# Performance work log

Hardware: AMD Instinct MI355X
Metric: run time of the kernel (lower is better)

## Reference

```python
import jax, jax.numpy as jnp
import numpy as np

B, N, H, E = 16, 10000, 128, 320000


def setup_inputs() -> dict:
    key = jax.random.key(0)
    k1, k2, k3, k4, k5 = jax.random.split(key, 5)
    node_embeddings = jax.random.normal(k1, (B, N, H), dtype=jnp.float32)
    missing_mask = jax.random.randint(k2, (B, N), 0, 2, dtype=jnp.int32)
    edge_index = jax.random.randint(k3, (2, E), 0, N, dtype=jnp.int32)
    W1 = jax.random.normal(k4, (2 * H, H), dtype=jnp.float32) * 0.02
    b1 = jnp.zeros((H,), dtype=jnp.float32)
    W2 = jax.random.normal(k5, (H, H), dtype=jnp.float32) * 0.02
    b2 = jnp.zeros((H,), dtype=jnp.float32)
    return {"node_embeddings": node_embeddings, "missing_mask": missing_mask,
            "edge_index": edge_index, "W1": W1, "b1": b1, "W2": W2, "b2": b2}


def reference(node_embeddings, missing_mask, edge_index, W1, b1, W2, b2):
    num_nodes = node_embeddings.shape[1]
    src, dst = edge_index[0], edge_index[1]
    # scatter-add of source embeddings into destination nodes, per batch
    msgs = node_embeddings[:, src, :]  # [B, E, H]
    neighbor = jax.vmap(
        lambda m: jax.ops.segment_sum(m, dst, num_segments=num_nodes)
    )(msgs)  # [B, N, H]
    # original divides by ones clamped to 1 -> identity, omitted
    context = jnp.concatenate([neighbor, node_embeddings], axis=-1)  # [B, N, 2H]
    h = jax.nn.relu(jnp.einsum('bnf,fh->bnh', context, W1) + b1)
    imputed = jnp.einsum('bnf,fh->bnh', h, W2) + b2
    mask = (missing_mask.astype(bool))[..., None]  # [B, N, 1]
    return jnp.where(mask, imputed, node_embeddings)
```

## Files before the change

kernel.cpp:

```cpp
#include <hip/hip_runtime.h>

#define B_ 16
#define N_ 10000
#define H_ 128
#define E_ 320000
#define R_ (B_ * N_)
#define LDC 264
#define NM_PAD 64

typedef __attribute__((ext_vector_type(8))) short bf16x8;
typedef __attribute__((ext_vector_type(4))) float f32x4;

static __device__ __forceinline__ unsigned short f2bf(float f) {
    unsigned int u = __float_as_uint(f);
    return (unsigned short)((u + 0x7fffu + ((u >> 16) & 1u)) >> 16);
}

__global__ __launch_bounds__(256) void cvt_bf16_kernel(const float4* __restrict__ in4,
                                                       uint4* __restrict__ out4) {
    int t = blockIdx.x * 256 + threadIdx.x;
    float4 a = in4[t * 2 + 0];
    float4 b = in4[t * 2 + 1];
    unsigned int r0 = f2bf(a.x), r1 = f2bf(a.y), r2 = f2bf(a.z), r3 = f2bf(a.w);
    unsigned int r4 = f2bf(b.x), r5 = f2bf(b.y), r6 = f2bf(b.z), r7 = f2bf(b.w);
    uint4 o;
    o.x = r0 | (r1 << 16);
    o.y = r2 | (r3 << 16);
    o.z = r4 | (r5 << 16);
    o.w = r6 | (r7 << 16);
    out4[t] = o;
}

__global__ __launch_bounds__(256) void wt1_kernel(const float* __restrict__ W,
                                                  unsigned short* __restrict__ Wt) {
    int idx = blockIdx.x * 256 + threadIdx.x;
    int n = idx >> 8, k = idx & 255;
    Wt[idx] = f2bf(W[k * 128 + n]);
}
__global__ __launch_bounds__(256) void wt2_kernel(const float* __restrict__ W,
                                                  unsigned short* __restrict__ Wt) {
    int idx = blockIdx.x * 256 + threadIdx.x;
    int n = idx >> 7, k = idx & 127;
    Wt[idx] = f2bf(W[k * 128 + n]);
}

__global__ void hist_kernel(const int* __restrict__ dst, int* __restrict__ counts) {
    int e = blockIdx.x * blockDim.x + threadIdx.x;
    if (e < E_) atomicAdd(&counts[dst[e]], 1);
}

__global__ __launch_bounds__(1024) void scan_kernel(const int* __restrict__ counts,
                                                    int* __restrict__ offsets,
                                                    int* __restrict__ cursor) {
    __shared__ int sums[1024];
    int t = threadIdx.x;
    const int chunk = (N_ + 1023) / 1024;
    int lo = t * chunk;
    int hi = min(lo + chunk, N_);
    int s = 0;
    for (int i = lo; i < hi; ++i) s += counts[i];
    sums[t] = s;
    __syncthreads();
    for (int off = 1; off < 1024; off <<= 1) {
        int add = (t >= off) ? sums[t - off] : 0;
        __syncthreads();
        sums[t] += add;
        __syncthreads();
    }
    int run = (t == 0) ? 0 : sums[t - 1];
    for (int i = lo; i < hi; ++i) {
        int c = counts[i];
        offsets[i] = run;
        cursor[i] = run;
        run += c;
    }
    if (t == 1023) offsets[N_] = run;
}

__global__ void fill_kernel(const int* __restrict__ src, const int* __restrict__ dst,
                            int* __restrict__ cursor, int* __restrict__ srcs_sorted) {
    int e = blockIdx.x * blockDim.x + threadIdx.x;
    if (e < E_) {
        int d = dst[e];
        int pos = atomicAdd(&cursor[d], 1);
        srcs_sorted[pos] = src[e];
    }
}

__global__ __launch_bounds__(256) void mcount_kernel(const int* __restrict__ mask,
                                                     int* __restrict__ blk_cnt) {
    int e = blockIdx.x * 256 + threadIdx.x;
    unsigned long long bal = __ballot(mask[e] != 0);
    __shared__ int wc[4];
    int wv = threadIdx.x >> 6;
    if ((threadIdx.x & 63) == 0) wc[wv] = __popcll(bal);
    __syncthreads();
    if (threadIdx.x == 0) blk_cnt[blockIdx.x] = wc[0] + wc[1] + wc[2] + wc[3];
}

__global__ __launch_bounds__(1024) void mscan_kernel(const int* __restrict__ blk_cnt,
                                                     int* __restrict__ blk_off,
                                                     int* __restrict__ nmbuf,
                                                     int* __restrict__ rows) {
    __shared__ int s[1024];
    int t = threadIdx.x;
    int v = (t < 625) ? blk_cnt[t] : 0;
    s[t] = v;
    __syncthreads();
    for (int off = 1; off < 1024; off <<= 1) {
        int add = (t >= off) ? s[t - off] : 0;
        __syncthreads();
        s[t] += add;
        __syncthreads();
    }
    if (t < 625) blk_off[t] = s[t] - v;
    int nm = s[1023];
    if (t == 0) nmbuf[0] = nm;
    if (t < NM_PAD) rows[nm + t] = 0;
}

__global__ __launch_bounds__(256) void mscatter_kernel(const int* __restrict__ mask,
                                                       const int* __restrict__ blk_off,
                                                       int* __restrict__ rows) {
    int e = blockIdx.x * 256 + threadIdx.x;
    int m = (mask[e] != 0);
    unsigned long long bal = __ballot(m);
    int lane = threadIdx.x & 63;
    int wv = threadIdx.x >> 6;
    __shared__ int wcnt[4];
    if (lane == 0) wcnt[wv] = __popcll(bal);
    __syncthreads();
    int woff = 0;
    for (int i = 0; i < wv; ++i) woff += wcnt[i];
    int rank = __popcll(bal & ((1ull << lane) - 1ull));
    if (m) rows[blk_off[blockIdx.x] + woff + rank] = e;
}

__global__ __launch_bounds__(256) void gather_c_kernel(
        const uint4* __restrict__ ebf4, const int* __restrict__ offsets,
        const int* __restrict__ srcs, const int* __restrict__ rows,
        const int* __restrict__ nmbuf, uint4* __restrict__ nbc4) {
    int bid = blockIdx.x;
    int lb = (bid & 7) * 1250 + (bid >> 3);
    int i = lb * 16 + (threadIdx.x >> 4);
    if (i >= nmbuf[0]) return;
    int r = rows[i];
    int b = r / N_;
    int n = r - b * N_;
    int lane = threadIdx.x & 15;
    int beg = offsets[n], end = offsets[n + 1];
    const uint4* sb = ebf4 + (size_t)b * N_ * 16;
    float acc[8] = {0.f, 0.f, 0.f, 0.f, 0.f, 0.f, 0.f, 0.f};
    for (int e = beg; e < end; ++e) {
        int s = srcs[e];
        uint4 v = sb[(size_t)s * 16 + lane];
        acc[0] += __uint_as_float(v.x << 16);
        acc[1] += __uint_as_float(v.x & 0xffff0000u);
        acc[2] += __uint_as_float(v.y << 16);
        acc[3] += __uint_as_float(v.y & 0xffff0000u);
        acc[4] += __uint_as_float(v.z << 16);
        acc[5] += __uint_as_float(v.z & 0xffff0000u);
        acc[6] += __uint_as_float(v.w << 16);
        acc[7] += __uint_as_float(v.w & 0xffff0000u);
    }
    unsigned int rr[8];
#pragma unroll
    for (int k = 0; k < 8; ++k) rr[k] = f2bf(acc[k]);
    uint4 o;
    o.x = rr[0] | (rr[1] << 16);
    o.y = rr[2] | (rr[3] << 16);
    o.z = rr[4] | (rr[5] << 16);
    o.w = rr[6] | (rr[7] << 16);
    nbc4[(size_t)i * 16 + lane] = o;
}

__global__ __launch_bounds__(256) void mlp_mfma_kernel(
        const uint4* __restrict__ nbc4,
        const uint4* __restrict__ ebf4,
        const int* __restrict__ rows, const int* __restrict__ nmbuf,
        const unsigned short* __restrict__ W1t,
        const unsigned short* __restrict__ W2t,
        const float* __restrict__ b1, const float* __restrict__ b2,
        float* __restrict__ out) {
    int nm = nmbuf[0];
    int tile = blockIdx.x * 64;
    if (tile >= nm) return;
    __shared__ unsigned short ctxb[64 * LDC];
    int tx = threadIdx.x;
    int lane = tx & 63;
    int w = tx >> 6;
    int l15 = lane & 15;
    int g = lane >> 4;

#pragma unroll
    for (int kk = 0; kk < 8; ++kk) {
        int q = tx + kk * 256;
        int row = q >> 5, c16 = q & 31;
        uint4 v;
        if (c16 < 16) v = nbc4[(size_t)(tile + row) * 16 + c16];
        else          v = ebf4[(size_t)rows[tile + row] * 16 + (c16 - 16)];
        *(uint4*)((char*)ctxb + row * (LDC * 2) + c16 * 16) = v;
    }
    __syncthreads();

    f32x4 acc[4][2];
#pragma unroll
    for (int rf = 0; rf < 4; ++rf)
#pragma unroll
        for (int nt = 0; nt < 2; ++nt) acc[rf][nt] = (f32x4){0.f, 0.f, 0.f, 0.f};
#pragma unroll
    for (int ks = 0; ks < 8; ++ks) {
        bf16x8 a[4];
#pragma unroll
        for (int rf = 0; rf < 4; ++rf)
            a[rf] = *(const bf16x8*)((const char*)ctxb + (rf * 16 + l15) * (LDC * 2) + (ks * 32 + g * 8) * 2);
#pragma unroll
        for (int nt = 0; nt < 2; ++nt) {
            bf16x8 bfrag = *(const bf16x8*)(W1t + (size_t)((2 * w + nt) * 16 + l15) * 256 + ks * 32 + g * 8);
#pragma unroll
            for (int rf = 0; rf < 4; ++rf)
                acc[rf][nt] = __builtin_amdgcn_mfma_f32_16x16x32_bf16(a[rf], bfrag, acc[rf][nt], 0, 0, 0);
        }
    }
    __syncthreads();

#pragma unroll
    for (int nt = 0; nt < 2; ++nt) {
        float bv = b1[(2 * w + nt) * 16 + l15];
#pragma unroll
        for (int rf = 0; rf < 4; ++rf)
#pragma unroll
            for (int reg = 0; reg < 4; ++reg) {
                int hrow = rf * 16 + 4 * g + reg;
                float hv = fmaxf(acc[rf][nt][reg] + bv, 0.f);
                ctxb[hrow * LDC + (2 * w + nt) * 16 + l15] = f2bf(hv);
            }
    }
    __syncthreads();

    f32x4 acc2[4][2];
#pragma unroll
    for (int rf = 0; rf < 4; ++rf)
#pragma unroll
        for (int nt = 0; nt < 2; ++nt) acc2[rf][nt] = (f32x4){0.f, 0.f, 0.f, 0.f};
#pragma unroll
    for (int ks = 0; ks < 4; ++ks) {
        bf16x8 a[4];
#pragma unroll
        for (int rf = 0; rf < 4; ++rf)
            a[rf] = *(const bf16x8*)((const char*)ctxb + (rf * 16 + l15) * (LDC * 2) + (ks * 32 + g * 8) * 2);
#pragma unroll
        for (int nt = 0; nt < 2; ++nt) {
            bf16x8 bfrag = *(const bf16x8*)(W2t + (size_t)((2 * w + nt) * 16 + l15) * 128 + ks * 32 + g * 8);
#pragma unroll
            for (int rf = 0; rf < 4; ++rf)
                acc2[rf][nt] = __builtin_amdgcn_mfma_f32_16x16x32_bf16(a[rf], bfrag, acc2[rf][nt], 0, 0, 0);
        }
    }

    float bv2[2];
#pragma unroll
    for (int nt = 0; nt < 2; ++nt) bv2[nt] = b2[(2 * w + nt) * 16 + l15];
#pragma unroll
    for (int rf = 0; rf < 4; ++rf)
#pragma unroll
        for (int reg = 0; reg < 4; ++reg) {
            int i = tile + rf * 16 + 4 * g + reg;
            if (i < nm) {
                size_t rb = (size_t)rows[i] * 128;
#pragma unroll
                for (int nt = 0; nt < 2; ++nt)
                    out[rb + (2 * w + nt) * 16 + l15] = acc2[rf][nt][reg] + bv2[nt];
            }
        }
}

extern "C" void kernel_launch(void* const* d_in, const int* in_sizes, int n_in,
                              void* d_out, int out_size, void* d_ws, size_t ws_size,
                              hipStream_t stream) {
    const float* emb  = (const float*)d_in[0];
    const int*   mask = (const int*)d_in[1];
    const int*   eidx = (const int*)d_in[2];
    const float* W1   = (const float*)d_in[3];
    const float* b1   = (const float*)d_in[4];
    const float* W2   = (const float*)d_in[5];
    const float* b2   = (const float*)d_in[6];
    float* out = (float*)d_out;

    const int* src = eidx;
    const int* dst = eidx + E_;

    char* ws = (char*)d_ws;
    size_t o = 0;
    unsigned short* ebf = (unsigned short*)(ws + o); o += (size_t)R_ * H_ * 2;
    unsigned short* nbc = (unsigned short*)(ws + o); o += (size_t)(R_ + NM_PAD) * H_ * 2;
    unsigned short* W1t = (unsigned short*)(ws + o); o += 128 * 256 * 2;
    unsigned short* W2t = (unsigned short*)(ws + o); o += 128 * 128 * 2;
    int* counts  = (int*)(ws + o);  o += 40064;
    int* offsets = (int*)(ws + o);  o += 40064;
    int* cursor  = (int*)(ws + o);  o += 40064;
    int* srcs    = (int*)(ws + o);  o += (size_t)E_ * 4;
    int* rows    = (int*)(ws + o);  o += (size_t)(R_ + NM_PAD) * 4;
    int* blk_cnt = (int*)(ws + o);  o += 2560;
    int* blk_off = (int*)(ws + o);  o += 2560;
    int* nmbuf   = (int*)(ws + o);  o += 64;

    hipMemcpyAsync(out, emb, (size_t)R_ * H_ * sizeof(float),
                   hipMemcpyDeviceToDevice, stream);

    hipMemsetAsync(counts, 0, N_ * sizeof(int), stream);
    cvt_bf16_kernel<<<R_ * H_ / (256 * 8), 256, 0, stream>>>(
        (const float4*)emb, (uint4*)ebf);
    wt1_kernel<<<128, 256, 0, stream>>>(W1, W1t);
    wt2_kernel<<<64, 256, 0, stream>>>(W2, W2t);
    hist_kernel<<<E_ / 256, 256, 0, stream>>>(dst, counts);
    scan_kernel<<<1, 1024, 0, stream>>>(counts, offsets, cursor);
    fill_kernel<<<E_ / 256, 256, 0, stream>>>(src, dst, cursor, srcs);
    mcount_kernel<<<R_ / 256, 256, 0, stream>>>(mask, blk_cnt);
    mscan_kernel<<<1, 1024, 0, stream>>>(blk_cnt, blk_off, nmbuf, rows);
    mscatter_kernel<<<R_ / 256, 256, 0, stream>>>(mask, blk_off, rows);
    gather_c_kernel<<<R_ / 16, 256, 0, stream>>>(
        (const uint4*)ebf, offsets, srcs, rows, nmbuf, (uint4*)nbc);
    mlp_mfma_kernel<<<R_ / 64, 256, 0, stream>>>(
        (const uint4*)nbc, (const uint4*)ebf, rows, nmbuf, W1t, W2t, b1, b2, out);
}
```

Measured before the change: 415.1 us.

## Fuse masked output copy into bf16 prep and split edge gather across wavefront

The full device-to-device copy of embeddings into the output is removed. The bf16 conversion kernel now also writes fp32 embeddings to the output, but only for rows whose mask is zero, which avoids writing rows the MLP later overwrites. The neighbor gather now gives each row a full 64-lane wavefront instead of 16 lanes. Four lanes groups take strided edges and are combined with cross-lane shuffles, which raises memory-level parallelism per row. The trade-off is four times as many blocks, idle lanes on low-degree rows, and a mask read in the prep kernel.

```diff
diff --git a/kernel.cpp b/kernel.cpp
--- a/kernel.cpp
+++ b/kernel.cpp
@@ -16,11 +16,13 @@
     return (unsigned short)((u + 0x7fffu + ((u >> 16) & 1u)) >> 16);
 }
 
-__global__ __launch_bounds__(256) void cvt_bf16_kernel(const float4* __restrict__ in4,
-                                                       uint4* __restrict__ out4) {
+__global__ __launch_bounds__(256) void prep_kernel(const float4* __restrict__ emb4,
+                                                   const int* __restrict__ mask,
+                                                   float4* __restrict__ out4,
+                                                   uint4* __restrict__ ebf4) {
     int t = blockIdx.x * 256 + threadIdx.x;
-    float4 a = in4[t * 2 + 0];
-    float4 b = in4[t * 2 + 1];
+    float4 a = emb4[t * 2 + 0];
+    float4 b = emb4[t * 2 + 1];
     unsigned int r0 = f2bf(a.x), r1 = f2bf(a.y), r2 = f2bf(a.z), r3 = f2bf(a.w);
     unsigned int r4 = f2bf(b.x), r5 = f2bf(b.y), r6 = f2bf(b.z), r7 = f2bf(b.w);
     uint4 o;
@@ -28,7 +30,12 @@
     o.y = r2 | (r3 << 16);
     o.z = r4 | (r5 << 16);
     o.w = r6 | (r7 << 16);
-    out4[t] = o;
+    ebf4[t] = o;
+    int row = t >> 4;
+    if (!mask[row]) {
+        out4[t * 2 + 0] = a;
+        out4[t * 2 + 1] = b;
+    }
 }
 
 __global__ __launch_bounds__(256) void wt1_kernel(const float* __restrict__ W,
@@ -140,20 +147,20 @@
         const uint4* __restrict__ ebf4, const int* __restrict__ offsets,
         const int* __restrict__ srcs, const int* __restrict__ rows,
         const int* __restrict__ nmbuf, uint4* __restrict__ nbc4) {
-    int bid = blockIdx.x;
-    int lb = (bid & 7) * 1250 + (bid >> 3);
-    int i = lb * 16 + (threadIdx.x >> 4);
+    int i = blockIdx.x * 4 + (threadIdx.x >> 6);
     if (i >= nmbuf[0]) return;
     int r = rows[i];
     int b = r / N_;
     int n = r - b * N_;
-    int lane = threadIdx.x & 15;
+    int lane = threadIdx.x & 63;
+    int f16 = lane & 15;
+    int way = lane >> 4;
     int beg = offsets[n], end = offsets[n + 1];
-    const uint4* sb = ebf4 + (size_t)b * N_ * 16;
+    const uint4* sb = ebf4 + (size_t)b * (N_ * 16);
     float acc[8] = {0.f, 0.f, 0.f, 0.f, 0.f, 0.f, 0.f, 0.f};
-    for (int e = beg; e < end; ++e) {
+    for (int e = beg + way; e < end; e += 4) {
         int s = srcs[e];
-        uint4 v = sb[(size_t)s * 16 + lane];
+        uint4 v = sb[(size_t)s * 16 + f16];
         acc[0] += __uint_as_float(v.x << 16);
         acc[1] += __uint_as_float(v.x & 0xffff0000u);
         acc[2] += __uint_as_float(v.y << 16);
@@ -163,15 +170,22 @@
         acc[6] += __uint_as_float(v.w << 16);
         acc[7] += __uint_as_float(v.w & 0xffff0000u);
     }
-    unsigned int rr[8];
-#pragma unroll
-    for (int k = 0; k < 8; ++k) rr[k] = f2bf(acc[k]);
-    uint4 o;
-    o.x = rr[0] | (rr[1] << 16);
-    o.y = rr[2] | (rr[3] << 16);
-    o.z = rr[4] | (rr[5] << 16);
-    o.w = rr[6] | (rr[7] << 16);
-    nbc4[(size_t)i * 16 + lane] = o;
+#pragma unroll
+    for (int k = 0; k < 8; ++k) {
+        acc[k] += __shfl_xor(acc[k], 16, 64);
+        acc[k] += __shfl_xor(acc[k], 32, 64);
+    }
+    if (way == 0) {
+        unsigned int rr[8];
+#pragma unroll
+        for (int k = 0; k < 8; ++k) rr[k] = f2bf(acc[k]);
+        uint4 o;
+        o.x = rr[0] | (rr[1] << 16);
+        o.y = rr[2] | (rr[3] << 16);
+        o.z = rr[4] | (rr[5] << 16);
+        o.w = rr[6] | (rr[7] << 16);
+        nbc4[(size_t)i * 16 + f16] = o;
+    }
 }
 
 __global__ __launch_bounds__(256) void mlp_mfma_kernel(
@@ -305,12 +319,9 @@
     int* blk_off = (int*)(ws + o);  o += 2560;
     int* nmbuf   = (int*)(ws + o);  o += 64;
 
-    hipMemcpyAsync(out, emb, (size_t)R_ * H_ * sizeof(float),
-                   hipMemcpyDeviceToDevice, stream);
-
     hipMemsetAsync(counts, 0, N_ * sizeof(int), stream);
-    cvt_bf16_kernel<<<R_ * H_ / (256 * 8), 256, 0, stream>>>(
-        (const float4*)emb, (uint4*)ebf);
+    prep_kernel<<<R_ * H_ / (256 * 8), 256, 0, stream>>>(
+        (const float4*)emb, mask, (float4*)out, (uint4*)ebf);
     wt1_kernel<<<128, 256, 0, stream>>>(W1, W1t);
     wt2_kernel<<<64, 256, 0, stream>>>(W2, W2t);
     hist_kernel<<<E_ / 256, 256, 0, stream>>>(dst, counts);
@@ -319,7 +330,7 @@
     mcount_kernel<<<R_ / 256, 256, 0, stream>>>(mask, blk_cnt);
     mscan_kernel<<<1, 1024, 0, stream>>>(blk_cnt, blk_off, nmbuf, rows);
     mscatter_kernel<<<R_ / 256, 256, 0, stream>>>(mask, blk_off, rows);
-    gather_c_kernel<<<R_ / 16, 256, 0, stream>>>(
+    gather_c_kernel<<<R_ / 4, 256, 0, stream>>>(
         (const uint4*)ebf, offsets, srcs, rows, nmbuf, (uint4*)nbc);
     mlp_mfma_kernel<<<R_ / 64, 256, 0, stream>>>(
         (const uint4*)nbc, (const uint4*)ebf, rows, nmbuf, W1t, W2t, b1, b2, out);
```

Measured after the change: 344.4 us. 1.21x faster.
